# Optimization experiments

Hardware: AMD Instinct MI355X
Metric: run time of the kernel (lower is better)

Reference implementation:

```python
import jax, jax.numpy as jnp
import numpy as np

N_NODES = 16000
N_EDGES = 256000
DIM = 256
HEADS = 8
DH = DIM // HEADS
BLOCKS = 3
EPS = 1e-5


def _ln_graph(x, g, b):
    # PyG LayerNorm, mode='graph', batch=None: scalar mean/std over ALL elements,
    # then per-channel affine.
    x = x - x.mean()
    x = x / (x.std() + EPS)
    return x * g + b


def _block(x, src, dst, x_edge, inv_dist, p):
    (Wq, bq, Wk, bk, Wv, bv, We, Ws, bs, g1, b1, W1, c1, W2, c2, g2, b2) = p
    # per-edge gather + projections  [E, H, DH]
    q = (x[dst] @ Wq + bq).reshape(N_EDGES, HEADS, DH)
    e = (x_edge @ We).reshape(N_EDGES, HEADS, DH)          # lin_edge (no bias)
    k = (x[src] @ Wk + bk).reshape(N_EDGES, HEADS, DH) + e
    # distance-scaled attention logits [E, H]
    alpha = (q * k).sum(-1) * (inv_dist[:, None] / np.sqrt(DH))
    # segment softmax over destination nodes (PyG softmax, +1e-16 in denom)
    amax = jax.ops.segment_max(alpha, dst, num_segments=N_NODES)
    ex = jnp.exp(alpha - amax[dst])
    denom = jax.ops.segment_sum(ex, dst, num_segments=N_NODES)
    attn = ex / (denom[dst] + 1e-16)
    v = (x[src] @ Wv + bv).reshape(N_EDGES, HEADS, DH) + e
    msg = (v * attn[:, :, None]).reshape(N_EDGES, DIM)      # concat heads
    out = jax.ops.segment_sum(msg, dst, num_segments=N_NODES)
    out = out + x @ Ws + bs                                 # root / skip weight
    x = _ln_graph(x + out, g1, b1)                          # mha residual + norm
    ffn = jnp.maximum(x @ W1 + c1, 0.0) @ W2 + c2           # 2-layer ReLU MLP
    return _ln_graph(x + ffn, g2, b2)


def setup_inputs() -> dict:
    key = jax.random.key(0)
    ks = jax.random.split(key, 16)
    s = 0.05
    B = BLOCKS

    def w(k, shape):
        return jax.random.normal(k, shape, jnp.float32) * s

    return {
        'x': jax.random.normal(ks[0], (N_NODES, DIM), jnp.float32),
        'edge_index': jax.random.randint(ks[1], (2, N_EDGES), 0, N_NODES),
        'x_edge': jax.random.normal(ks[2], (N_EDGES, DIM), jnp.float32),
        'x_dist': jax.random.uniform(ks[3], (N_EDGES,), jnp.float32, 1.0, 5.0),
        'Wq': w(ks[4], (B, DIM, DIM)), 'bq': jnp.zeros((B, DIM), jnp.float32),
        'Wk': w(ks[5], (B, DIM, DIM)), 'bk': jnp.zeros((B, DIM), jnp.float32),
        'Wv': w(ks[6], (B, DIM, DIM)), 'bv': jnp.zeros((B, DIM), jnp.float32),
        'We': w(ks[7], (B, DIM, DIM)),
        'Wskip': w(ks[8], (B, DIM, DIM)), 'bskip': jnp.zeros((B, DIM), jnp.float32),
        'ln1_g': jnp.ones((B, DIM), jnp.float32), 'ln1_b': jnp.zeros((B, DIM), jnp.float32),
        'W1': w(ks[9], (B, DIM, 4 * DIM)), 'bf1': jnp.zeros((B, 4 * DIM), jnp.float32),
        'W2': w(ks[10], (B, 4 * DIM, DIM)), 'bf2': jnp.zeros((B, DIM), jnp.float32),
        'ln2_g': jnp.ones((B, DIM), jnp.float32), 'ln2_b': jnp.zeros((B, DIM), jnp.float32),
    }


def reference(x, edge_index, x_edge, x_dist, Wq, bq, Wk, bk, Wv, bv, We,
              Wskip, bskip, ln1_g, ln1_b, W1, bf1, W2, bf2, ln2_g, ln2_b):
    src, dst = edge_index[0], edge_index[1]  # PyG: x_j = x[src], x_i = x[dst]
    inv_dist = 1.0 / x_dist
    for i in range(BLOCKS):
        p = (Wq[i], bq[i], Wk[i], bk[i], Wv[i], bv[i], We[i], Wskip[i], bskip[i],
             ln1_g[i], ln1_b[i], W1[i], bf1[i], W2[i], bf2[i], ln2_g[i], ln2_b[i])
        x = _block(x, src, dst, x_edge, inv_dist, p)
    return x
```

## Files before the change

kernel.cpp:

```cpp
#include <hip/hip_runtime.h>
#include <hip/hip_bf16.h>
#include <cstddef>

#define N_NODES 16000
#define N_EDGES 256000
#define DIM 256
#define HEADS 8
#define DFF 1024
#define LN_EPS 1e-5f
#define CNT ((float)((size_t)N_NODES * DIM))
#define RSDH 0.17677669529663687f

typedef __attribute__((ext_vector_type(8))) short short8;
typedef __attribute__((ext_vector_type(4))) float floatx4;

__device__ __forceinline__ float bf2f(unsigned int s) {
    return __uint_as_float(s << 16);
}

__device__ __forceinline__ float2 ln_ms(const float* __restrict__ s) {
    float mu = s[0] * (1.0f / CNT);
    float var = s[1] * (1.0f / CNT) - mu * mu;
    float2 r; r.x = mu; r.y = 1.0f / (sqrtf(fmaxf(var, 0.0f)) + LN_EPS);
    return r;
}

__device__ __forceinline__ void async16(const __hip_bfloat16* g, __hip_bfloat16* l) {
    __builtin_amdgcn_global_load_lds(
        (const __attribute__((address_space(1))) void*)g,
        (__attribute__((address_space(3))) void*)l, 16, 0, 0);
}

__device__ __forceinline__ void pack8(__hip_bfloat16* d, float4 a, float4 b) {
    union { short8 f; __hip_bfloat16 h[8]; } u;
    u.h[0] = __float2bfloat16(a.x); u.h[1] = __float2bfloat16(a.y);
    u.h[2] = __float2bfloat16(a.z); u.h[3] = __float2bfloat16(a.w);
    u.h[4] = __float2bfloat16(b.x); u.h[5] = __float2bfloat16(b.y);
    u.h[6] = __float2bfloat16(b.z); u.h[7] = __float2bfloat16(b.w);
    *(short8*)d = u.f;
}

__device__ __forceinline__ float4 lnaff(float4 v, float4 g, float4 b, float mu, float sc) {
    v.x = (v.x - mu) * sc * g.x + b.x;
    v.y = (v.y - mu) * sc * g.y + b.y;
    v.z = (v.z - mu) * sc * g.z + b.z;
    v.w = (v.w - mu) * sc * g.w + b.w;
    return v;
}

template<int BIAS, int RELU, int RES, int OBF16, int ACVT, int TM>
__global__ __launch_bounds__(256) void mgemm_k(
    const void* __restrict__ Ap, const __hip_bfloat16* __restrict__ Bt,
    const float* __restrict__ bias, const float* __restrict__ res,
    void* __restrict__ C, void* __restrict__ C2, int M, int K, int N,
    const float* __restrict__ lnA_s, const float* __restrict__ lnA_g,
    const float* __restrict__ lnA_b,
    const float* __restrict__ lnR_s, const float* __restrict__ lnR_g,
    const float* __restrict__ lnR_b,
    float* __restrict__ ostats)
{
    __shared__ __hip_bfloat16 As[TM * 32];
    __shared__ __hip_bfloat16 Bs[128 * 32];
    __shared__ float rs[8];
    const int tid = threadIdx.x;
    const int lane = tid & 63, wv = tid >> 6;
    const int wm = (TM == 128) ? (wv & 1) * 64 : 0;
    const int wn = (TM == 128) ? (wv >> 1) * 64 : wv * 32;
    const int NJ = (TM == 128) ? 4 : 2;
    const int row0 = blockIdx.y * TM, col0 = blockIdx.x * 128;
    const int lr = tid >> 2;
    const int lk = (tid & 3) * 8;

    float muA = 0.0f, scA = 1.0f;
    if (ACVT && lnA_s) { float2 t = ln_ms(lnA_s); muA = t.x; scA = t.y; }

    floatx4 acc[4][4];
    const floatx4 zf = {0.f, 0.f, 0.f, 0.f};
    #pragma unroll
    for (int i = 0; i < 4; i++)
        #pragma unroll
        for (int j = 0; j < 4; j++) acc[i][j] = zf;

    const int a_fo = (wm + (lane & 15)) * 32 + (lane >> 4) * 8;
    const int b_fo = (wn + (lane & 15)) * 32 + (lane >> 4) * 8;

    for (int k0 = 0; k0 < K; k0 += 32) {
        if (ACVT) {
            const float* A = (const float*)Ap;
            const float* p0 = A + (size_t)(row0 + lr) * K + k0 + lk;
            float4 v0 = *(const float4*)(p0);
            float4 v1 = *(const float4*)(p0 + 4);
            if (lnA_s) {
                float4 ga = *(const float4*)(lnA_g + k0 + lk);
                float4 gb = *(const float4*)(lnA_g + k0 + lk + 4);
                float4 ba = *(const float4*)(lnA_b + k0 + lk);
                float4 bb = *(const float4*)(lnA_b + k0 + lk + 4);
                v0 = lnaff(v0, ga, ba, muA, scA);
                v1 = lnaff(v1, gb, bb, muA, scA);
                if (TM == 128) {
                    const float* p1 = A + (size_t)(row0 + lr + 64) * K + k0 + lk;
                    float4 w0 = lnaff(*(const float4*)(p1), ga, ba, muA, scA);
                    float4 w1 = lnaff(*(const float4*)(p1 + 4), gb, bb, muA, scA);
                    pack8(As + 2048 + tid * 8, w0, w1);
                }
            } else if (TM == 128) {
                const float* p1 = A + (size_t)(row0 + lr + 64) * K + k0 + lk;
                pack8(As + 2048 + tid * 8, *(const float4*)(p1), *(const float4*)(p1 + 4));
            }
            pack8(As + tid * 8, v0, v1);
        } else {
            const __hip_bfloat16* A = (const __hip_bfloat16*)Ap;
            async16(A + (size_t)(row0 + lr) * K + k0 + lk, As + tid * 8);
            if (TM == 128)
                async16(A + (size_t)(row0 + lr + 64) * K + k0 + lk, As + 2048 + tid * 8);
        }
        async16(Bt + (size_t)(col0 + lr) * K + k0 + lk, Bs + tid * 8);
        async16(Bt + (size_t)(col0 + lr + 64) * K + k0 + lk, Bs + 2048 + tid * 8);
        __syncthreads();
        short8 a[4], b[4];
        #pragma unroll
        for (int i = 0; i < 4; i++)
            a[i] = *(const short8*)(As + a_fo + i * 16 * 32);
        #pragma unroll
        for (int j = 0; j < NJ; j++)
            b[j] = *(const short8*)(Bs + b_fo + j * 16 * 32);
        #pragma unroll
        for (int i = 0; i < 4; i++)
            #pragma unroll
            for (int j = 0; j < NJ; j++)
                acc[i][j] = __builtin_amdgcn_mfma_f32_16x16x32_bf16(a[i], b[j], acc[i][j], 0, 0, 0);
        __syncthreads();
    }
    float muR = 0.0f, scR = 1.0f;
    if (RES && lnR_s) { float2 t = ln_ms(lnR_s); muR = t.x; scR = t.y; }
    const int rbase = row0 + wm + (lane >> 4) * 4;
    const int cbase = col0 + wn + (lane & 15);
    float s1 = 0.0f, s2 = 0.0f;
    #pragma unroll
    for (int j = 0; j < NJ; j++) {
        const int c = cbase + j * 16;
        float bb = BIAS ? bias[c] : 0.0f;
        float gr = (RES && lnR_s) ? lnR_g[c] : 1.0f;
        float br = (RES && lnR_s) ? lnR_b[c] : 0.0f;
        #pragma unroll
        for (int i = 0; i < 4; i++) {
            #pragma unroll
            for (int r = 0; r < 4; r++) {
                const int rr = rbase + i * 16 + r;
                float v = acc[i][j][r] + bb;
                if (RELU) v = fmaxf(v, 0.0f);
                if (RES) {
                    float rv = res[(size_t)rr * N + c];
                    if (lnR_s) rv = (rv - muR) * scR * gr + br;
                    v += rv;
                }
                if (ostats) { s1 += v; s2 += v * v; }
                if (OBF16 == 3) {
                    if (c < 512) {
                        ((float*)C)[(size_t)rr * 512 + c] = v;
                    } else {
                        const int cc = c - 512;
                        const int ccc = cc & 255;
                        const int idx = ((ccc >> 2) << 3) + (ccc & 3) + ((cc >> 8) << 2);
                        ((__hip_bfloat16*)C2)[(size_t)rr * 512 + idx] = __float2bfloat16(v);
                    }
                } else if (OBF16 == 1) {
                    ((__hip_bfloat16*)C)[(size_t)rr * N + c] = __float2bfloat16(v);
                } else {
                    ((float*)C)[(size_t)rr * N + c] = v;
                }
            }
        }
    }
    if (ostats) {
        #pragma unroll
        for (int o = 32; o > 0; o >>= 1) {
            s1 += __shfl_down(s1, o);
            s2 += __shfl_down(s2, o);
        }
        if (lane == 0) { rs[wv] = s1; rs[4 + wv] = s2; }
        __syncthreads();
        if (tid == 0) {
            atomicAdd(&ostats[0], rs[0] + rs[1] + rs[2] + rs[3]);
            atomicAdd(&ostats[1], rs[4] + rs[5] + rs[6] + rs[7]);
        }
    }
}

__global__ __launch_bounds__(256) void tcvt_k(const float* __restrict__ src,
                                              __hip_bfloat16* __restrict__ dst,
                                              int R, int C, int sStride, int dStride)
{
    src += (size_t)blockIdx.z * sStride;
    dst += (size_t)blockIdx.z * dStride;
    __shared__ float t[32][33];
    const int c0 = blockIdx.x * 32, r0 = blockIdx.y * 32;
    const int tx = threadIdx.x & 31, ty = threadIdx.x >> 5;
    #pragma unroll
    for (int j = 0; j < 32; j += 8)
        t[ty + j][tx] = src[(size_t)(r0 + ty + j) * C + c0 + tx];
    __syncthreads();
    #pragma unroll
    for (int j = 0; j < 32; j += 8)
        dst[(size_t)(c0 + ty + j) * R + r0 + tx] = __float2bfloat16(t[tx][ty + j]);
}

__global__ __launch_bounds__(256) void bcat_k(const float* __restrict__ ba,
                                              const float* __restrict__ bb,
                                              const float* __restrict__ bc,
                                              const float* __restrict__ bd,
                                              float* __restrict__ o)
{
    const int z = blockIdx.y;
    int t = blockIdx.x * 256 + threadIdx.x;
    float v = (t < 256) ? ba[z * 256 + t] : (t < 512) ? bb[z * 256 + t - 256]
            : (t < 768) ? bc[z * 256 + t - 512] : bd[z * 256 + t - 768];
    o[(size_t)z * 1024 + t] = v;
}

__global__ __launch_bounds__(256) void hist_k(const int* __restrict__ dst, int* __restrict__ deg)
{
    int e = blockIdx.x * blockDim.x + threadIdx.x;
    if (e < N_EDGES) atomicAdd(&deg[dst[e]], 1);
}

__global__ __launch_bounds__(1024) void scan_k(const int* __restrict__ deg,
                                               int* __restrict__ rowptr,
                                               int* __restrict__ cursor)
{
    __shared__ int wsum[16];
    const int t = threadIdx.x;
    const int base = t * 16;
    int local[16];
    int s = 0;
    if (t < 1000) {
        #pragma unroll
        for (int j = 0; j < 16; j++) { local[j] = s; s += deg[base + j]; }
    }
    const int lane = t & 63, w = t >> 6;
    int v = s;
    #pragma unroll
    for (int off = 1; off < 64; off <<= 1) {
        int u = __shfl_up(v, off);
        if (lane >= off) v += u;
    }
    if (lane == 63) wsum[w] = v;
    __syncthreads();
    if (t == 0) {
        int r = 0;
        #pragma unroll
        for (int i = 0; i < 16; i++) { int u = wsum[i]; wsum[i] = r; r += u; }
    }
    __syncthreads();
    const int excl = v - s + wsum[w];
    if (t < 1000) {
        #pragma unroll
        for (int j = 0; j < 16; j++) {
            rowptr[base + j] = excl + local[j];
            cursor[base + j] = excl + local[j];
        }
        if (t == 999) rowptr[16000] = excl + s;
    }
}

__global__ __launch_bounds__(256) void scatter_k(const int* __restrict__ dst,
                                                 const int* __restrict__ src,
                                                 const float* __restrict__ xd,
                                                 int* __restrict__ cursor,
                                                 int* __restrict__ eperm,
                                                 int* __restrict__ srcp,
                                                 float* __restrict__ scale)
{
    int e = blockIdx.x * blockDim.x + threadIdx.x;
    if (e < N_EDGES) {
        int pos = atomicAdd(&cursor[dst[e]], 1);
        eperm[pos] = e;
        srcp[pos] = src[e];
        scale[pos] = RSDH / xd[e];
    }
}

__global__ __launch_bounds__(256) void eprep_k(const float* __restrict__ xe,
                                               const int* __restrict__ eperm,
                                               __hip_bfloat16* __restrict__ xeb)
{
    const int r = blockIdx.x * 4 + (threadIdx.x >> 6);
    const int lane = threadIdx.x & 63;
    const int e = eperm[r];
    float4 v = *(const float4*)(xe + (size_t)e * DIM + lane * 4);
    union { short4 s; __hip_bfloat16 h[4]; } u;
    u.h[0] = __float2bfloat16(v.x); u.h[1] = __float2bfloat16(v.y);
    u.h[2] = __float2bfloat16(v.z); u.h[3] = __float2bfloat16(v.w);
    *(short4*)(xeb + (size_t)r * DIM + lane * 4) = u.s;
}

__global__ __launch_bounds__(256) void node_agg_k(
    const float* __restrict__ qs, const __hip_bfloat16* __restrict__ kvb,
    const __hip_bfloat16* __restrict__ Ep,
    const int* __restrict__ srcp, const float* __restrict__ scale,
    const int* __restrict__ rowptr,
    const float* __restrict__ xsrc, const float* __restrict__ lnx_s,
    const float* __restrict__ lnx_g, const float* __restrict__ lnx_b,
    float* __restrict__ y, float* __restrict__ ostats)
{
    __shared__ float rs[8];
    const int lane = threadIdx.x & 63;
    const int wv = threadIdx.x >> 6;
    const int n = blockIdx.x * 4 + wv;
    const float4 q = *(const float4*)(qs + (size_t)n * 512 + lane * 4);
    float ax0[4], ax1[4], ax2[4], ax3[4], den[4];
    #pragma unroll
    for (int t = 0; t < 4; t++) { ax0[t] = 0; ax1[t] = 0; ax2[t] = 0; ax3[t] = 0; den[t] = 0; }
    const int beg = rowptr[n], end = rowptr[n + 1];
    if (beg < end) {
        const int last = end - 1;
        uint4 kv[4]; uint2 eb[4]; float sc[4]; int sn[4];
        #pragma unroll
        for (int t = 0; t < 4; t++) {
            const int idx = min(beg + t, last);
            const int s = srcp[idx];
            kv[t] = *(const uint4*)(kvb + (size_t)s * 512 + lane * 8);
            eb[t] = *(const uint2*)(Ep + (size_t)idx * DIM + lane * 4);
            sc[t] = scale[idx];
        }
        #pragma unroll
        for (int t = 0; t < 4; t++)
            sn[t] = srcp[min(beg + 4 + t, last)];
        for (int i = beg; i < end; i += 4) {
            uint4 ckv[4]; uint2 ceb[4]; float csc[4];
            #pragma unroll
            for (int t = 0; t < 4; t++) { ckv[t] = kv[t]; ceb[t] = eb[t]; csc[t] = sc[t]; }
            if (i + 4 < end) {
                #pragma unroll
                for (int t = 0; t < 4; t++) {
                    const int idx = min(i + 4 + t, last);
                    kv[t] = *(const uint4*)(kvb + (size_t)sn[t] * 512 + lane * 8);
                    eb[t] = *(const uint2*)(Ep + (size_t)idx * DIM + lane * 4);
                    sc[t] = scale[idx];
                }
                #pragma unroll
                for (int t = 0; t < 4; t++)
                    sn[t] = srcp[min(i + 8 + t, last)];
            }
            float p[4];
            #pragma unroll
            for (int t = 0; t < 4; t++) {
                const float e0 = bf2f(ceb[t].x & 0xffffu), e1 = bf2f(ceb[t].x >> 16);
                const float e2 = bf2f(ceb[t].y & 0xffffu), e3 = bf2f(ceb[t].y >> 16);
                p[t] = q.x * (bf2f(ckv[t].x & 0xffffu) + e0)
                     + q.y * (bf2f(ckv[t].x >> 16) + e1)
                     + q.z * (bf2f(ckv[t].y & 0xffffu) + e2)
                     + q.w * (bf2f(ckv[t].y >> 16) + e3);
            }
            #pragma unroll
            for (int t = 0; t < 4; t++) p[t] += __shfl_xor(p[t], 1);
            #pragma unroll
            for (int t = 0; t < 4; t++) p[t] += __shfl_xor(p[t], 2);
            #pragma unroll
            for (int t = 0; t < 4; t++) p[t] += __shfl_xor(p[t], 4);
            #pragma unroll
            for (int t = 0; t < 4; t++) {
                const float ex = (i + t < end) ? __expf(p[t] * csc[t]) : 0.0f;
                den[t] += ex;
                const float e0 = bf2f(ceb[t].x & 0xffffu), e1 = bf2f(ceb[t].x >> 16);
                const float e2 = bf2f(ceb[t].y & 0xffffu), e3 = bf2f(ceb[t].y >> 16);
                ax0[t] = fmaf(bf2f(ckv[t].z & 0xffffu) + e0, ex, ax0[t]);
                ax1[t] = fmaf(bf2f(ckv[t].z >> 16) + e1, ex, ax1[t]);
                ax2[t] = fmaf(bf2f(ckv[t].w & 0xffffu) + e2, ex, ax2[t]);
                ax3[t] = fmaf(bf2f(ckv[t].w >> 16) + e3, ex, ax3[t]);
            }
        }
    }
    const float dn = 1.0f / (den[0] + den[1] + den[2] + den[3] + 1e-16f);
    const float a0 = ax0[0] + ax0[1] + ax0[2] + ax0[3];
    const float a1 = ax1[0] + ax1[1] + ax1[2] + ax1[3];
    const float a2 = ax2[0] + ax2[1] + ax2[2] + ax2[3];
    const float a3 = ax3[0] + ax3[1] + ax3[2] + ax3[3];
    const size_t o = (size_t)n * DIM + lane * 4;
    float4 xr = *(const float4*)(xsrc + o);
    if (lnx_s) {
        float2 t = ln_ms(lnx_s);
        const float4 g4 = *(const float4*)(lnx_g + lane * 4);
        const float4 b4 = *(const float4*)(lnx_b + lane * 4);
        xr = lnaff(xr, g4, b4, t.x, t.y);
    }
    const float4 sr = *(const float4*)(qs + (size_t)n * 512 + 256 + lane * 4);
    float4 out;
    out.x = xr.x + a0 * dn + sr.x;
    out.y = xr.y + a1 * dn + sr.y;
    out.z = xr.z + a2 * dn + sr.z;
    out.w = xr.w + a3 * dn + sr.w;
    *(float4*)(y + o) = out;
    float s1 = out.x + out.y + out.z + out.w;
    float s2 = out.x * out.x + out.y * out.y + out.z * out.z + out.w * out.w;
    #pragma unroll
    for (int of = 32; of > 0; of >>= 1) {
        s1 += __shfl_down(s1, of);
        s2 += __shfl_down(s2, of);
    }
    if (lane == 0) { rs[wv] = s1; rs[4 + wv] = s2; }
    __syncthreads();
    if (threadIdx.x == 0) {
        atomicAdd(&ostats[0], rs[0] + rs[1] + rs[2] + rs[3]);
        atomicAdd(&ostats[1], rs[4] + rs[5] + rs[6] + rs[7]);
    }
}

__global__ __launch_bounds__(256) void apply_k(
    const float* __restrict__ y, const float* __restrict__ stats,
    const float* __restrict__ g, const float* __restrict__ b,
    float* __restrict__ xo)
{
    int idx = blockIdx.x * blockDim.x + threadIdx.x;
    float2 t = ln_ms(stats);
    int cb = (idx & 63) * 4;
    float4 v  = *(const float4*)(y + (size_t)idx * 4);
    float4 gv = *(const float4*)(g + cb);
    float4 bv = *(const float4*)(b + cb);
    *(float4*)(xo + (size_t)idx * 4) = lnaff(v, gv, bv, t.x, t.y);
}

extern "C" void kernel_launch(void* const* d_in, const int* in_sizes, int n_in,
                              void* d_out, int out_size, void* d_ws, size_t ws_size,
                              hipStream_t stream) {
    const float* x_in   = (const float*)d_in[0];
    const int*   ei     = (const int*)d_in[1];
    const int*   src    = ei;
    const int*   dstp   = ei + N_EDGES;
    const float* x_edge = (const float*)d_in[2];
    const float* x_dist = (const float*)d_in[3];
    const float* Wq  = (const float*)d_in[4];
    const float* bq  = (const float*)d_in[5];
    const float* Wk  = (const float*)d_in[6];
    const float* bk  = (const float*)d_in[7];
    const float* Wv  = (const float*)d_in[8];
    const float* bv  = (const float*)d_in[9];
    const float* We  = (const float*)d_in[10];
    const float* Wsk = (const float*)d_in[11];
    const float* bsk = (const float*)d_in[12];
    const float* g1  = (const float*)d_in[13];
    const float* b1  = (const float*)d_in[14];
    const float* W1  = (const float*)d_in[15];
    const float* c1  = (const float*)d_in[16];
    const float* W2  = (const float*)d_in[17];
    const float* c2  = (const float*)d_in[18];
    const float* g2  = (const float*)d_in[19];
    const float* b2  = (const float*)d_in[20];

    char* p = (char*)d_ws;
    float* ybuf = (float*)p; p += (size_t)N_NODES * DIM * sizeof(float);
    float* qsb  = (float*)p; p += (size_t)N_NODES * 512 * sizeof(float);
    __hip_bfloat16* kvb = (__hip_bfloat16*)p; p += (size_t)N_NODES * 512 * 2;
    __hip_bfloat16* hb16 = (__hip_bfloat16*)p; p += (size_t)N_NODES * 1024 * 2;
    __hip_bfloat16* Ep   = (__hip_bfloat16*)p; p += (size_t)N_EDGES * DIM * 2;
    __hip_bfloat16* xeb  = (__hip_bfloat16*)p; p += (size_t)N_EDGES * DIM * 2;
    __hip_bfloat16* WqkvsT = (__hip_bfloat16*)p; p += (size_t)3 * 1024 * 256 * 2;
    __hip_bfloat16* WeT    = (__hip_bfloat16*)p; p += (size_t)3 * 256 * 256 * 2;
    __hip_bfloat16* W1T    = (__hip_bfloat16*)p; p += (size_t)3 * 1024 * 256 * 2;
    __hip_bfloat16* W2T    = (__hip_bfloat16*)p; p += (size_t)3 * 256 * 1024 * 2;
    float* bqkvs = (float*)p; p += (size_t)3 * 1024 * sizeof(float);
    float* stats = (float*)p;  p += 64;
    int* deg     = (int*)p;    p += (size_t)N_NODES * sizeof(int);
    int* rowptr  = (int*)p;    p += (size_t)(N_NODES + 4) * sizeof(int);
    int* cursor  = (int*)p;    p += (size_t)N_NODES * sizeof(int);
    int* eperm   = (int*)p;    p += (size_t)N_EDGES * sizeof(int);
    int* srcp    = (int*)p;    p += (size_t)N_EDGES * sizeof(int);
    float* scale = (float*)p;  p += (size_t)N_EDGES * sizeof(float);

    const dim3 blk(256);

    hipMemsetAsync(deg, 0, (size_t)N_NODES * sizeof(int), stream);
    hipMemsetAsync(stats, 0, 48, stream);
    hist_k<<<N_EDGES / 256, blk, 0, stream>>>(dstp, deg);
    scan_k<<<1, 1024, 0, stream>>>(deg, rowptr, cursor);
    scatter_k<<<N_EDGES / 256, blk, 0, stream>>>(dstp, src, x_dist, cursor, eperm, srcp, scale);
    eprep_k<<<N_EDGES / 4, blk, 0, stream>>>(x_edge, eperm, xeb);

    tcvt_k<<<dim3(8, 8, 3), blk, 0, stream>>>(Wq,  WqkvsT + 0 * 65536, 256, 256, 65536, 262144);
    tcvt_k<<<dim3(8, 8, 3), blk, 0, stream>>>(Wsk, WqkvsT + 1 * 65536, 256, 256, 65536, 262144);
    tcvt_k<<<dim3(8, 8, 3), blk, 0, stream>>>(Wk,  WqkvsT + 2 * 65536, 256, 256, 65536, 262144);
    tcvt_k<<<dim3(8, 8, 3), blk, 0, stream>>>(Wv,  WqkvsT + 3 * 65536, 256, 256, 65536, 262144);
    tcvt_k<<<dim3(8, 8, 3), blk, 0, stream>>>(We,  WeT, 256, 256, 65536, 65536);
    tcvt_k<<<dim3(32, 8, 3), blk, 0, stream>>>(W1, W1T, 256, 1024, 262144, 262144);
    tcvt_k<<<dim3(8, 32, 3), blk, 0, stream>>>(W2, W2T, 1024, 256, 262144, 262144);
    bcat_k<<<dim3(4, 3), blk, 0, stream>>>(bq, bsk, bk, bv, bqkvs);

    for (int i = 0; i < 3; i++) {
        const size_t bo = (size_t)i * DIM;
        const size_t b1o = (size_t)i * DFF;
        float* ln1 = stats + (size_t)i * 4;
        float* ln2 = stats + (size_t)i * 4 + 2;
        const float* pls = (i == 0) ? nullptr : stats + (size_t)(i - 1) * 4 + 2;
        const float* plg = (i == 0) ? nullptr : g2 + (size_t)(i - 1) * 256;
        const float* plb = (i == 0) ? nullptr : b2 + (size_t)(i - 1) * 256;
        const float* xsrc = (i == 0) ? x_in : ybuf;

        mgemm_k<1,0,0,3,1,128><<<dim3(8, 125), blk, 0, stream>>>(
            xsrc, WqkvsT + (size_t)i * 262144, bqkvs + (size_t)i * 1024, nullptr,
            qsb, kvb, N_NODES, DIM, 1024, pls, plg, plb, nullptr, nullptr, nullptr, nullptr);
        mgemm_k<0,0,0,1,0,128><<<dim3(2, 2000), blk, 0, stream>>>(
            xeb, WeT + (size_t)i * 65536, nullptr, nullptr,
            Ep, nullptr, N_EDGES, DIM, DIM, nullptr, nullptr, nullptr, nullptr, nullptr, nullptr, nullptr);
        node_agg_k<<<N_NODES / 4, blk, 0, stream>>>(qsb, kvb, Ep, srcp, scale, rowptr,
                                                    xsrc, pls, plg, plb, ybuf, ln1);
        mgemm_k<1,1,0,1,1,128><<<dim3(8, 125), blk, 0, stream>>>(
            ybuf, W1T + (size_t)i * 262144, c1 + b1o, nullptr,
            hb16, nullptr, N_NODES, DIM, DFF, ln1, g1 + bo, b1 + bo, nullptr, nullptr, nullptr, nullptr);
        mgemm_k<1,0,1,0,0,64><<<dim3(2, 250), blk, 0, stream>>>(
            hb16, W2T + (size_t)i * 262144, c2 + bo, ybuf,
            ybuf, nullptr, N_NODES, DFF, DIM, nullptr, nullptr, nullptr, ln1, g1 + bo, b1 + bo, ln2);
        if (i == 2)
            apply_k<<<(N_NODES * DIM) / 1024, blk, 0, stream>>>(
                ybuf, ln2, g2 + bo, b2 + bo, (float*)d_out);
    }
}
```

Baseline: 1.503 ms.

## Fuse edge-feature projection GEMM into node aggregation kernel

Removes the separate x_edge @ We GEMM and its bf16 Ep intermediate buffer. The aggregation kernel now handles 8 destination nodes per 512-thread block. It loads each 64-edge chunk of sorted edge features into swizzled LDS, computes the projection with MFMA, writes the result back to LDS, and then runs the softmax-weighted accumulation reading e from LDS. This avoids writing and re-reading the 256000x256 edge projection through global memory, at the cost of 32KB LDS per block, extra barriers, and serialising per-edge work within each wave.

```diff
diff --git a/kernel.cpp b/kernel.cpp
--- a/kernel.cpp
+++ b/kernel.cpp
@@ -294,89 +294,100 @@
     *(short4*)(xeb + (size_t)r * DIM + lane * 4) = u.s;
 }
 
-__global__ __launch_bounds__(256) void node_agg_k(
+__global__ __launch_bounds__(512) void nagg_f_k(
     const float* __restrict__ qs, const __hip_bfloat16* __restrict__ kvb,
-    const __hip_bfloat16* __restrict__ Ep,
+    const __hip_bfloat16* __restrict__ xeb, const __hip_bfloat16* __restrict__ WeT,
     const int* __restrict__ srcp, const float* __restrict__ scale,
     const int* __restrict__ rowptr,
     const float* __restrict__ xsrc, const float* __restrict__ lnx_s,
     const float* __restrict__ lnx_g, const float* __restrict__ lnx_b,
     float* __restrict__ y, float* __restrict__ ostats)
 {
-    __shared__ float rs[8];
-    const int lane = threadIdx.x & 63;
-    const int wv = threadIdx.x >> 6;
-    const int n = blockIdx.x * 4 + wv;
-    const float4 q = *(const float4*)(qs + (size_t)n * 512 + lane * 4);
-    float ax0[4], ax1[4], ax2[4], ax3[4], den[4];
-    #pragma unroll
-    for (int t = 0; t < 4; t++) { ax0[t] = 0; ax1[t] = 0; ax2[t] = 0; ax3[t] = 0; den[t] = 0; }
-    const int beg = rowptr[n], end = rowptr[n + 1];
-    if (beg < end) {
-        const int last = end - 1;
-        uint4 kv[4]; uint2 eb[4]; float sc[4]; int sn[4];
-        #pragma unroll
-        for (int t = 0; t < 4; t++) {
-            const int idx = min(beg + t, last);
-            const int s = srcp[idx];
-            kv[t] = *(const uint4*)(kvb + (size_t)s * 512 + lane * 8);
-            eb[t] = *(const uint2*)(Ep + (size_t)idx * DIM + lane * 4);
-            sc[t] = scale[idx];
-        }
-        #pragma unroll
-        for (int t = 0; t < 4; t++)
-            sn[t] = srcp[min(beg + 4 + t, last)];
-        for (int i = beg; i < end; i += 4) {
-            uint4 ckv[4]; uint2 ceb[4]; float csc[4];
+    __shared__ __hip_bfloat16 Axe[64 * 256];
+    __shared__ float rs[16];
+    const int tid = threadIdx.x, lane = tid & 63, wv = tid >> 6;
+    const int n0 = blockIdx.x * 8;
+    const int nn = n0 + wv;
+    const int e0 = rowptr[n0], eT = rowptr[n0 + 8];
+    const int begw = rowptr[nn], endw = rowptr[nn + 1];
+    const float4 q = *(const float4*)(qs + (size_t)nn * 512 + lane * 4);
+    float a0 = 0, a1 = 0, a2 = 0, a3 = 0, den = 0;
+    const __hip_bfloat16* wb0 = WeT + (size_t)(wv * 32 + (lane & 15)) * 256 + (lane >> 4) * 8;
+
+    for (int c0 = e0; c0 < eT; c0 += 64) {
+        #pragma unroll
+        for (int j = 0; j < 4; j++) {
+            const int cid = tid + 512 * j;
+            const int m = cid >> 5;
+            const int sl = (cid & 31) ^ (m & 7);
+            const int row = min(c0 + m, eT - 1);
+            async16(xeb + (size_t)row * 256 + sl * 8, Axe + cid * 8);
+        }
+        __syncthreads();
+        floatx4 ea[4][2];
+        const floatx4 zf = {0.f, 0.f, 0.f, 0.f};
+        #pragma unroll
+        for (int i = 0; i < 4; i++) { ea[i][0] = zf; ea[i][1] = zf; }
+        for (int k0 = 0; k0 < 256; k0 += 32) {
+            short8 a[4], b[2];
             #pragma unroll
-            for (int t = 0; t < 4; t++) { ckv[t] = kv[t]; ceb[t] = eb[t]; csc[t] = sc[t]; }
-            if (i + 4 < end) {
-                #pragma unroll
-                for (int t = 0; t < 4; t++) {
-                    const int idx = min(i + 4 + t, last);
-                    kv[t] = *(const uint4*)(kvb + (size_t)sn[t] * 512 + lane * 8);
-                    eb[t] = *(const uint2*)(Ep + (size_t)idx * DIM + lane * 4);
-                    sc[t] = scale[idx];
-                }
-                #pragma unroll
-                for (int t = 0; t < 4; t++)
-                    sn[t] = srcp[min(i + 8 + t, last)];
-            }
-            float p[4];
-            #pragma unroll
-            for (int t = 0; t < 4; t++) {
-                const float e0 = bf2f(ceb[t].x & 0xffffu), e1 = bf2f(ceb[t].x >> 16);
-                const float e2 = bf2f(ceb[t].y & 0xffffu), e3 = bf2f(ceb[t].y >> 16);
-                p[t] = q.x * (bf2f(ckv[t].x & 0xffffu) + e0)
-                     + q.y * (bf2f(ckv[t].x >> 16) + e1)
-                     + q.z * (bf2f(ckv[t].y & 0xffffu) + e2)
-                     + q.w * (bf2f(ckv[t].y >> 16) + e3);
+            for (int i = 0; i < 4; i++) {
+                const int m = (lane & 15) + 16 * i;
+                a[i] = *(const short8*)(Axe + m * 256 +
+                        ((((k0 >> 3) + (lane >> 4)) ^ (m & 7)) << 3));
             }
             #pragma unroll
-            for (int t = 0; t < 4; t++) p[t] += __shfl_xor(p[t], 1);
+            for (int j = 0; j < 2; j++)
+                b[j] = *(const short8*)(wb0 + j * 4096 + k0);
             #pragma unroll
-            for (int t = 0; t < 4; t++) p[t] += __shfl_xor(p[t], 2);
+            for (int i = 0; i < 4; i++)
+                #pragma unroll
+                for (int j = 0; j < 2; j++)
+                    ea[i][j] = __builtin_amdgcn_mfma_f32_16x16x32_bf16(a[i], b[j], ea[i][j], 0, 0, 0);
+        }
+        __syncthreads();
+        #pragma unroll
+        for (int i = 0; i < 4; i++)
             #pragma unroll
-            for (int t = 0; t < 4; t++) p[t] += __shfl_xor(p[t], 4);
-            #pragma unroll
-            for (int t = 0; t < 4; t++) {
-                const float ex = (i + t < end) ? __expf(p[t] * csc[t]) : 0.0f;
-                den[t] += ex;
-                const float e0 = bf2f(ceb[t].x & 0xffffu), e1 = bf2f(ceb[t].x >> 16);
-                const float e2 = bf2f(ceb[t].y & 0xffffu), e3 = bf2f(ceb[t].y >> 16);
-                ax0[t] = fmaf(bf2f(ckv[t].z & 0xffffu) + e0, ex, ax0[t]);
-                ax1[t] = fmaf(bf2f(ckv[t].z >> 16) + e1, ex, ax1[t]);
-                ax2[t] = fmaf(bf2f(ckv[t].w & 0xffffu) + e2, ex, ax2[t]);
-                ax3[t] = fmaf(bf2f(ckv[t].w >> 16) + e3, ex, ax3[t]);
-            }
-        }
-    }
-    const float dn = 1.0f / (den[0] + den[1] + den[2] + den[3] + 1e-16f);
-    const float a0 = ax0[0] + ax0[1] + ax0[2] + ax0[3];
-    const float a1 = ax1[0] + ax1[1] + ax1[2] + ax1[3];
-    const float a2 = ax2[0] + ax2[1] + ax2[2] + ax2[3];
-    const float a3 = ax3[0] + ax3[1] + ax3[2] + ax3[3];
-    const size_t o = (size_t)n * DIM + lane * 4;
+            for (int j = 0; j < 2; j++)
+                #pragma unroll
+                for (int r = 0; r < 4; r++) {
+                    const int m = i * 16 + (lane >> 4) * 4 + r;
+                    const int col = wv * 32 + j * 16 + (lane & 15);
+                    *(__hip_bfloat16*)((char*)Axe + m * 512 + ((col * 2) ^ ((m & 7) << 4))) =
+                        __float2bfloat16(ea[i][j][r]);
+                }
+        __syncthreads();
+        const int lo = max(begw, c0), hi = min(endw, c0 + 64);
+        int s = (lo < hi) ? srcp[lo] : 0;
+        for (int idx = lo; idx < hi; idx++) {
+            const int scur = s;
+            if (idx + 1 < hi) s = srcp[idx + 1];
+            const float sc = scale[idx];
+            const uint4 kv = *(const uint4*)(kvb + (size_t)scur * 512 + lane * 8);
+            const int el = idx - c0;
+            const uint2 eb = *(const uint2*)((const char*)Axe + el * 512 +
+                                             ((lane * 8) ^ ((el & 7) << 4)));
+            const float e0v = bf2f(eb.x & 0xffffu), e1v = bf2f(eb.x >> 16);
+            const float e2v = bf2f(eb.y & 0xffffu), e3v = bf2f(eb.y >> 16);
+            float part = q.x * (bf2f(kv.x & 0xffffu) + e0v)
+                       + q.y * (bf2f(kv.x >> 16) + e1v)
+                       + q.z * (bf2f(kv.y & 0xffffu) + e2v)
+                       + q.w * (bf2f(kv.y >> 16) + e3v);
+            part += __shfl_xor(part, 1);
+            part += __shfl_xor(part, 2);
+            part += __shfl_xor(part, 4);
+            const float ex = __expf(part * sc);
+            den += ex;
+            a0 = fmaf(bf2f(kv.z & 0xffffu) + e0v, ex, a0);
+            a1 = fmaf(bf2f(kv.z >> 16) + e1v, ex, a1);
+            a2 = fmaf(bf2f(kv.w & 0xffffu) + e2v, ex, a2);
+            a3 = fmaf(bf2f(kv.w >> 16) + e3v, ex, a3);
+        }
+        __syncthreads();
+    }
+    const float dn = 1.0f / (den + 1e-16f);
+    const size_t o = (size_t)nn * DIM + lane * 4;
     float4 xr = *(const float4*)(xsrc + o);
     if (lnx_s) {
         float2 t = ln_ms(lnx_s);
@@ -384,7 +395,7 @@
         const float4 b4 = *(const float4*)(lnx_b + lane * 4);
         xr = lnaff(xr, g4, b4, t.x, t.y);
     }
-    const float4 sr = *(const float4*)(qs + (size_t)n * 512 + 256 + lane * 4);
+    const float4 sr = *(const float4*)(qs + (size_t)nn * 512 + 256 + lane * 4);
     float4 out;
     out.x = xr.x + a0 * dn + sr.x;
     out.y = xr.y + a1 * dn + sr.y;
@@ -398,11 +409,11 @@
         s1 += __shfl_down(s1, of);
         s2 += __shfl_down(s2, of);
     }
-    if (lane == 0) { rs[wv] = s1; rs[4 + wv] = s2; }
+    if (lane == 0) { rs[wv] = s1; rs[8 + wv] = s2; }
     __syncthreads();
-    if (threadIdx.x == 0) {
-        atomicAdd(&ostats[0], rs[0] + rs[1] + rs[2] + rs[3]);
-        atomicAdd(&ostats[1], rs[4] + rs[5] + rs[6] + rs[7]);
+    if (tid == 0) {
+        atomicAdd(&ostats[0], rs[0] + rs[1] + rs[2] + rs[3] + rs[4] + rs[5] + rs[6] + rs[7]);
+        atomicAdd(&ostats[1], rs[8] + rs[9] + rs[10] + rs[11] + rs[12] + rs[13] + rs[14] + rs[15]);
     }
 }
 
@@ -452,7 +463,6 @@
     float* qsb  = (float*)p; p += (size_t)N_NODES * 512 * sizeof(float);
     __hip_bfloat16* kvb = (__hip_bfloat16*)p; p += (size_t)N_NODES * 512 * 2;
     __hip_bfloat16* hb16 = (__hip_bfloat16*)p; p += (size_t)N_NODES * 1024 * 2;
-    __hip_bfloat16* Ep   = (__hip_bfloat16*)p; p += (size_t)N_EDGES * DIM * 2;
     __hip_bfloat16* xeb  = (__hip_bfloat16*)p; p += (size_t)N_EDGES * DIM * 2;
     __hip_bfloat16* WqkvsT = (__hip_bfloat16*)p; p += (size_t)3 * 1024 * 256 * 2;
     __hip_bfloat16* WeT    = (__hip_bfloat16*)p; p += (size_t)3 * 256 * 256 * 2;
@@ -498,11 +508,9 @@
         mgemm_k<1,0,0,3,1,128><<<dim3(8, 125), blk, 0, stream>>>(
             xsrc, WqkvsT + (size_t)i * 262144, bqkvs + (size_t)i * 1024, nullptr,
             qsb, kvb, N_NODES, DIM, 1024, pls, plg, plb, nullptr, nullptr, nullptr, nullptr);
-        mgemm_k<0,0,0,1,0,128><<<dim3(2, 2000), blk, 0, stream>>>(
-            xeb, WeT + (size_t)i * 65536, nullptr, nullptr,
-            Ep, nullptr, N_EDGES, DIM, DIM, nullptr, nullptr, nullptr, nullptr, nullptr, nullptr, nullptr);
-        node_agg_k<<<N_NODES / 4, blk, 0, stream>>>(qsb, kvb, Ep, srcp, scale, rowptr,
-                                                    xsrc, pls, plg, plb, ybuf, ln1);
+        nagg_f_k<<<N_NODES / 8, dim3(512), 0, stream>>>(
+            qsb, kvb, xeb, WeT + (size_t)i * 65536, srcp, scale, rowptr,
+            xsrc, pls, plg, plb, ybuf, ln1);
         mgemm_k<1,1,0,1,1,128><<<dim3(8, 125), blk, 0, stream>>>(
             ybuf, W1T + (size_t)i * 262144, c1 + b1o, nullptr,
             hb16, nullptr, N_NODES, DIM, DFF, ln1, g1 + bo, b1 + bo, nullptr, nullptr, nullptr, nullptr);
```

Result: slower. 1.643 ms (+9.3%).
